# Kernel tuning notes

Hardware: AMD Instinct MI355X
Metric: run time of the kernel (lower is better)

The kernel has to match this reference:

```python
import jax, jax.numpy as jnp
import numpy as np

B, S, D = 4, 1024, 1024
H, DH = 16, 64          # num_heads, attention_dim_per_head = attention_dim // num_heads
BIAS_DIM = 64
N_BIAS = 16384          # number of sparse relative-bias entries
NEG_MIN = jnp.finfo(jnp.float32).min


def setup_inputs() -> dict:
    key = jax.random.key(0)
    ks = jax.random.split(key, 12)
    states = jax.random.normal(ks[0], (B, S, D), dtype=jnp.float32)
    key_states = jax.random.normal(ks[1], (B, S, D), dtype=jnp.float32)
    masks = jnp.ones((B, 1, S, S), dtype=jnp.float32)
    # attention_bias columns: (batch_idx, q_idx, k_idx, bias_id)
    bi = jax.random.randint(ks[2], (N_BIAS,), 0, B)
    qi = jax.random.randint(ks[3], (N_BIAS,), 0, S)
    ki = jax.random.randint(ks[4], (N_BIAS,), 0, S)
    ei = jax.random.randint(ks[5], (N_BIAS,), 0, BIAS_DIM)
    attention_bias = jnp.stack([bi, qi, ki, ei], axis=1).astype(jnp.int32)
    # glorot-ish scaled weights
    def glorot(k, shape, fan_in, fan_out):
        lim = np.sqrt(6.0 / (fan_in + fan_out))
        return jax.random.uniform(k, shape, jnp.float32, -lim, lim)
    Wq = glorot(ks[6], (D, H, DH), D, H * DH)
    Wk = glorot(ks[7], (D, H, DH), D, H * DH)
    Wv = glorot(ks[8], (D, H, DH), D, H * DH)
    Wo = glorot(ks[9], (H, DH, D), H * DH, D)
    bias_embs = glorot(ks[10], (BIAS_DIM, DH), BIAS_DIM, DH)
    bias_scalar = glorot(ks[11], (DH, 1), DH, 1)
    return {"states": states, "key_states": key_states, "masks": masks,
            "attention_bias": attention_bias, "Wq": Wq, "Wk": Wk, "Wv": Wv,
            "Wo": Wo, "bias_embs": bias_embs, "bias_scalar": bias_scalar}


def reference(states, key_states, masks, attention_bias, Wq, Wk, Wv, Wo, bias_embs, bias_scalar):
    # QKV projections: btd,dha->btha
    q = jnp.einsum('btd,dha->btha', states, Wq)
    k = jnp.einsum('btd,dha->btha', key_states, Wk)
    v = jnp.einsum('btd,dha->btha', key_states, Wv)
    # raw scores [B,H,Q,K]
    alpha = jnp.einsum('bkha,bqha->bhqk', k, q)
    # sparse relative bias: one_hot @ bias_embs == gather; @ bias_scalar -> scalar per entry
    k_red = jnp.sum(k, axis=-1)                                   # [B,K,H]
    bias_vals = (bias_embs[attention_bias[:, -1]] @ bias_scalar)[:, 0]  # [N]
    bqk = jnp.zeros((alpha.shape[0], alpha.shape[2], alpha.shape[3]), dtype=alpha.dtype)
    # tf.scatter_nd sums duplicate indices -> .at[...].add
    bqk = bqk.at[attention_bias[:, 0], attention_bias[:, 1], attention_bias[:, 2]].add(bias_vals)
    alpha = alpha + jnp.einsum('bqk,bkh->bhqk', bqk, k_red)
    alpha = alpha * jax.lax.rsqrt(jnp.float32(DH))
    alpha = alpha * masks + (1.0 - jnp.ceil(masks)) * NEG_MIN
    alpha = jax.nn.softmax(alpha, axis=-1)
    alpha = alpha * masks
    context = jnp.einsum('bhqk,bkha->bqha', alpha, v)
    return jnp.einsum('btha,had->btd', context, Wo)
```

## Files before the change

### kernel.cpp

```cpp
#include <hip/hip_runtime.h>
#include <stdint.h>


typedef __attribute__((ext_vector_type(8))) short short8;
typedef __attribute__((ext_vector_type(4))) float f32x4;
typedef __attribute__((ext_vector_type(4))) unsigned short ushort4v;
typedef __attribute__((ext_vector_type(2))) unsigned uint2v;
typedef __attribute__((ext_vector_type(4))) unsigned uint4v;

#define DEVI __device__ __forceinline__

constexpr float NEG_MIN = -3.4028234663852886e38f;
constexpr float LOG2E   = 1.4426950408889634f;

DEVI unsigned short f2b(float f) {
    union { float f; unsigned u; } x; x.f = f;
    unsigned u = x.u;
    unsigned r = (u + 0x7fffu + ((u >> 16) & 1u)) >> 16;
    return (unsigned short)r;
}
DEVI float hi_as_f(unsigned p) { union { unsigned u; float f; } x; x.u = p & 0xffff0000u; return x.f; }
DEVI float lo_as_f(unsigned p) { union { unsigned u; float f; } x; x.u = p << 16; return x.f; }
DEVI float asf(unsigned u) { union { unsigned u; float f; } x; x.u = u; return x.f; }

DEVI void gl_lds16(const unsigned short* g, unsigned short* l) {
    __builtin_amdgcn_global_load_lds(
        (const __attribute__((address_space(1))) unsigned int*)g,
        (__attribute__((address_space(3))) unsigned int*)l, 16, 0, 0);
}

DEVI short8 ldswz(const unsigned short* base, int row, int slot) {
    return *reinterpret_cast<const short8*>(
        reinterpret_cast<const char*>(base) + row * 128 + (((slot ^ row) & 7) << 4));
}

__global__ void __launch_bounds__(256) prep_kernel(const float* __restrict__ s0,
                                                   const float* __restrict__ s1,
                                                   const float* __restrict__ Wq,
                                                   const float* __restrict__ Wk,
                                                   const float* __restrict__ Wv,
                                                   const float* __restrict__ Wo,
                                                   unsigned short* __restrict__ d0,
                                                   unsigned short* __restrict__ d1,
                                                   unsigned short* __restrict__ Wqt,
                                                   unsigned short* __restrict__ Wot) {
    __shared__ float t[64][65];
    int bid = blockIdx.x, tid = threadIdx.x;
    if (bid < 8192) {
        int i = bid * 256 + tid;
        const float* src = (i < 1024 * 1024) ? s0 : s1;
        unsigned short* dst = (i < 1024 * 1024) ? d0 : d1;
        int j = i & (1024 * 1024 - 1);
        float4 v = reinterpret_cast<const float4*>(src)[j];
        ushort4v o;
        o.x = f2b(v.x); o.y = f2b(v.y); o.z = f2b(v.z); o.w = f2b(v.w);
        reinterpret_cast<ushort4v*>(dst)[j] = o;
        return;
    }
    int wb = bid - 8192;
    int wi = wb >> 8, sub = wb & 255;
    const float* src = (wi == 0) ? Wq : ((wi == 1) ? Wk : ((wi == 2) ? Wv : Wo));
    unsigned short* dst = (wi == 3) ? Wot : (Wqt + (size_t)wi * 1024 * 1024);
    float scale = (wi == 0) ? 0.125f : 1.0f;
    const int R = 1024, C = 1024;
    int bc = sub & 15, br = sub >> 4;
    int r0 = tid >> 4, c4 = (tid & 15) << 2;
    for (int i = 0; i < 4; ++i) {
        int row = r0 + i * 16;
        float4 v = *reinterpret_cast<const float4*>(&src[(size_t)(br * 64 + row) * C + bc * 64 + c4]);
        t[row][c4] = v.x; t[row][c4 + 1] = v.y; t[row][c4 + 2] = v.z; t[row][c4 + 3] = v.w;
    }
    __syncthreads();
    int cr0 = tid >> 4, r4 = (tid & 15) << 2;
    for (int i = 0; i < 4; ++i) {
        int crow = cr0 + i * 16;
        ushort4v o;
        o.x = f2b(t[r4][crow] * scale); o.y = f2b(t[r4 + 1][crow] * scale);
        o.z = f2b(t[r4 + 2][crow] * scale); o.w = f2b(t[r4 + 3][crow] * scale);
        *reinterpret_cast<ushort4v*>(&dst[(size_t)(bc * 64 + crow) * R + br * 64 + r4]) = o;
    }
}

template <int OUT_F32, int DO_KRED>
DEVI void gemm128_body(const unsigned short* __restrict__ A,
                       const unsigned short* __restrict__ Bt,
                       void* __restrict__ Cv, int bm, int bn,
                       unsigned short* As, unsigned short* Bs,
                       float* __restrict__ kredT) {
    const int Kd = 1024, N = 1024;
    int tid = threadIdx.x, l = tid & 63, w = tid >> 6;
    int wm = w >> 1, wn = w & 1;
    int l15 = l & 15, l16 = l >> 4;
    f32x4 acc[4][4] = {};
    int lr = l >> 3, ls = l & 7;
    int gcol = ((ls ^ (lr & 7)) << 3);
    const unsigned short* Ag = A + (size_t)(bm * 128 + w * 8 + lr) * Kd + gcol;
    const unsigned short* Bg = Bt + (size_t)(bn * 128 + w * 8 + lr) * Kd + gcol;
    unsigned short* AsW = As + (w * 8) * 64;
    unsigned short* BsW = Bs + (w * 8) * 64;
    for (int kt = 0; kt < Kd; kt += 64) {
        __syncthreads();
#pragma unroll
        for (int i = 0; i < 4; ++i) {
            gl_lds16(Ag + kt + (size_t)(i * 32) * Kd, AsW + i * 32 * 64);
            gl_lds16(Bg + kt + (size_t)(i * 32) * Kd, BsW + i * 32 * 64);
        }
        __syncthreads();
#pragma unroll
        for (int h = 0; h < 2; ++h) {
            short8 af[4], bf[4];
#pragma unroll
            for (int m = 0; m < 4; ++m)
                af[m] = ldswz(As, wm * 64 + m * 16 + l15, h * 4 + l16);
#pragma unroll
            for (int n = 0; n < 4; ++n)
                bf[n] = ldswz(Bs, wn * 64 + n * 16 + l15, h * 4 + l16);
#pragma unroll
            for (int m = 0; m < 4; ++m)
#pragma unroll
                for (int n = 0; n < 4; ++n)
                    acc[m][n] = __builtin_amdgcn_mfma_f32_16x16x32_bf16(af[m], bf[n], acc[m][n], 0, 0, 0);
        }
    }
#pragma unroll
    for (int m = 0; m < 4; ++m)
#pragma unroll
        for (int n = 0; n < 4; ++n)
#pragma unroll
            for (int r = 0; r < 4; ++r) {
                int row = bm * 128 + wm * 64 + m * 16 + ((l >> 4) << 2) + r;
                int col = bn * 128 + wn * 64 + n * 16 + l15;
                float v = acc[m][n][r];
                if (OUT_F32) reinterpret_cast<float*>(Cv)[(size_t)row * N + col] = v;
                else reinterpret_cast<unsigned short*>(Cv)[(size_t)row * N + col] = f2b(v);
            }
    if (DO_KRED) {
        int hw = bn * 2 + wn;
#pragma unroll
        for (int m = 0; m < 4; ++m) {
            f32x4 rs = (acc[m][0] + acc[m][1]) + (acc[m][2] + acc[m][3]);
#pragma unroll
            for (int d = 1; d < 16; d <<= 1) {
                f32x4 t;
                t[0] = __shfl_xor(rs[0], d); t[1] = __shfl_xor(rs[1], d);
                t[2] = __shfl_xor(rs[2], d); t[3] = __shfl_xor(rs[3], d);
                rs += t;
            }
            if (l15 == 0) {
#pragma unroll
                for (int r = 0; r < 4; ++r) {
                    int row = bm * 128 + wm * 64 + m * 16 + ((l >> 4) << 2) + r;
                    kredT[((size_t)((row >> 10) * 16 + hw) << 10) + (row & 1023)] = rs[r] * 0.125f;
                }
            }
        }
    }
}

__global__ void __launch_bounds__(256) gemm_qkv(const unsigned short* __restrict__ Sb,
                                                const unsigned short* __restrict__ Kb,
                                                const unsigned short* __restrict__ W3,
                                                unsigned short* __restrict__ Qb,
                                                unsigned short* __restrict__ Kbf,
                                                unsigned short* __restrict__ Vb,
                                                float* __restrict__ kredT) {
    __shared__ unsigned short As[128 * 64];
    __shared__ unsigned short Bs[128 * 64];
    int g = blockIdx.x >> 8, sub = blockIdx.x & 255;
    const unsigned short* A = (g == 0) ? Sb : Kb;
    const unsigned short* Bt = W3 + (size_t)g * (1024 * 1024);
    unsigned short* C = (g == 0) ? Qb : ((g == 1) ? Kbf : Vb);
    if (g == 1)
        gemm128_body<0, 1>(A, Bt, C, sub >> 3, sub & 7, As, Bs, kredT);
    else
        gemm128_body<0, 0>(A, Bt, C, sub >> 3, sub & 7, As, Bs, nullptr);
}

__global__ void __launch_bounds__(256) gemm_wo(const unsigned short* __restrict__ A,
                                               const unsigned short* __restrict__ Bt,
                                               float* __restrict__ C) {
    __shared__ unsigned short As[128 * 64];
    __shared__ unsigned short Bs[128 * 64];
    gemm128_body<1, 0>(A, Bt, C, blockIdx.x >> 3, blockIdx.x & 7, As, Bs, nullptr);
}

__global__ void __launch_bounds__(256) zero_tv(float* __restrict__ bqkT,
                                               const unsigned short* __restrict__ V,
                                               unsigned short* __restrict__ Vt) {
    __shared__ unsigned short t[64][66];
    int bid = blockIdx.x, tid = threadIdx.x;
    if (bid < 4096) {
        float4 z = {0.f, 0.f, 0.f, 0.f};
        reinterpret_cast<float4*>(bqkT)[bid * 256 + tid] = z;
        return;
    }
    int vb = bid - 4096;
    int st = vb & 15, h = (vb >> 4) & 15, b = vb >> 8;
    int s = tid >> 2, c16 = (tid & 3) << 4;
    const unsigned short* src = V + ((size_t)((b * 1024 + st * 64 + s) * 16 + h)) * 64 + c16;
    short8 v0 = *reinterpret_cast<const short8*>(src);
    short8 v1 = *reinterpret_cast<const short8*>(src + 8);
    for (int j = 0; j < 8; ++j) {
        t[s][c16 + j] = (unsigned short)v0[j];
        t[s][c16 + 8 + j] = (unsigned short)v1[j];
    }
    __syncthreads();
    int a = tid >> 2, s16 = (tid & 3) << 4;
    short8 o0, o1;
    for (int j = 0; j < 8; ++j) {
        o0[j] = (short)t[s16 + j][a];
        o1[j] = (short)t[s16 + 8 + j][a];
    }
    unsigned short* dst = Vt + ((size_t)((b * 16 + h) * 64 + a)) * 1024 + st * 64 + s16;
    *reinterpret_cast<short8*>(dst) = o0;
    *reinterpret_cast<short8*>(dst + 8) = o1;
}

__global__ void __launch_bounds__(256) scatter_bias(const int* __restrict__ ab,
                                                    const float* __restrict__ embs,
                                                    const float* __restrict__ scal,
                                                    float* __restrict__ pk2f, int n) {
    __shared__ float tab[64];
    int tid = threadIdx.x;
    if (tid < 64) {
        float v = 0.f;
        for (int a = 0; a < 64; ++a) v += embs[tid * 64 + a] * scal[a];
        tab[tid] = v;
    }
    __syncthreads();
    int i = blockIdx.x * 256 + tid;
    if (i >= n) return;
    int4 e = *reinterpret_cast<const int4*>(&ab[i * 4]);
    size_t idx = (((size_t)(e.x * 16 + (e.z >> 6)) * 1024) + e.y) * 64 + (e.z & 63);
    atomicAdd(&pk2f[idx], tab[e.w]);
}

__global__ void __launch_bounds__(256) pack_T(const float* __restrict__ masks,
                                              unsigned* __restrict__ pk2) {
    __shared__ float mt[64][65];
    int bid = blockIdx.x;
    int qb = bid & 15, kt = (bid >> 4) & 15, b = bid >> 8;
    int tid = threadIdx.x;
    int ql = tid >> 2, c = tid & 3;
    const float* mrow = masks + ((size_t)(b * 1024 + qb * 64 + ql)) * 1024 + kt * 64 + c * 16;
#pragma unroll
    for (int j = 0; j < 4; ++j) {
        float4 v = *reinterpret_cast<const float4*>(mrow + j * 4);
        mt[ql][c * 16 + j * 4 + 0] = v.x; mt[ql][c * 16 + j * 4 + 1] = v.y;
        mt[ql][c * 16 + j * 4 + 2] = v.z; mt[ql][c * 16 + j * 4 + 3] = v.w;
    }
    __syncthreads();
    unsigned* orow = pk2 + (((size_t)(b * 16 + kt) * 1024) + qb * 64 + ql) * 64 + c * 16;
#pragma unroll
    for (int j = 0; j < 4; ++j) {
        uint4v bv = *reinterpret_cast<const uint4v*>(orow + j * 4);
        uint4v o;
        o.x = ((unsigned)f2b(mt[ql][c * 16 + j * 4 + 0]) << 16) | f2b(asf(bv.x));
        o.y = ((unsigned)f2b(mt[ql][c * 16 + j * 4 + 1]) << 16) | f2b(asf(bv.y));
        o.z = ((unsigned)f2b(mt[ql][c * 16 + j * 4 + 2]) << 16) | f2b(asf(bv.z));
        o.w = ((unsigned)f2b(mt[ql][c * 16 + j * 4 + 3]) << 16) | f2b(asf(bv.w));
        *reinterpret_cast<uint4v*>(orow + j * 4) = o;
    }
}

__global__ void __launch_bounds__(256, 4) attn_kernel(const unsigned short* __restrict__ Q,
                                                      const unsigned short* __restrict__ K,
                                                      const unsigned short* __restrict__ Vt,
                                                      const unsigned* __restrict__ pk2,
                                                      const float* __restrict__ kredT,
                                                      unsigned short* __restrict__ ctx) {
    __shared__ __align__(16) unsigned short Ks[64 * 64];
    __shared__ __align__(16) unsigned short Vs[64 * 64];
    __shared__ __align__(16) unsigned short p_s[4][16][72];

    int bid = blockIdx.x;
    int g = bid & 63, qb = bid >> 6;
    int b = g >> 4, h = g & 15;
    int tid = threadIdx.x, w = tid >> 6, l = tid & 63;
    int qbase = qb * 64 + w * 16;
    int l15 = l & 15, l16 = l >> 4, koff = l16 << 3;

    int srow = tid >> 3, sslot = tid & 7;
    int sbyte = srow * 128 + (((sslot ^ srow) & 7) << 4);

    const unsigned short* Kg = K + ((size_t)b << 20) + h * 64 + sslot * 8;
    const unsigned short* Vg = Vt + ((size_t)(b * 16 + h) << 16) + (size_t)srow * 1024 + sslot * 8;
    const unsigned* pkp = pk2 + ((size_t)b << 20) + (size_t)(qbase + l15) * 64 + (l16 << 2);
    const float* krp = kredT + ((size_t)(b * 16 + h) << 10);

    short8 qf0, qf1;
    {
        const unsigned short* qp = Q + ((size_t)((b * 1024 + qbase + l15) * 16 + h)) * 64 + koff;
        qf0 = *reinterpret_cast<const short8*>(qp);
        qf1 = *reinterpret_cast<const short8*>(qp + 32);
    }

    short8 kpre0 = *reinterpret_cast<const short8*>(Kg + (size_t)srow * 1024);
    short8 kpre1 = *reinterpret_cast<const short8*>(Kg + (size_t)(srow + 32) * 1024);
    short8 vpre0 = *reinterpret_cast<const short8*>(Vg);
    short8 vpre1 = *reinterpret_cast<const short8*>(Vg + (size_t)32 * 1024);
    uint4v pku[4];
#pragma unroll
    for (int n = 0; n < 4; ++n) pku[n] = *reinterpret_cast<const uint4v*>(pkp + n * 16);
    f32x4 kr4[4];
#pragma unroll
    for (int n = 0; n < 4; ++n)
        kr4[n] = *reinterpret_cast<const f32x4*>(&krp[n * 16 + (l16 << 2)]);

    float m_r = -INFINITY, l_r = 0.f;
    f32x4 O[4] = {};

    for (int kt = 0; kt < 16; ++kt) {
        int kbase = kt * 64;

        __syncthreads();
        *reinterpret_cast<short8*>(reinterpret_cast<char*>(Ks) + sbyte) = kpre0;
        *reinterpret_cast<short8*>(reinterpret_cast<char*>(Ks) + 32 * 128 + sbyte) = kpre1;
        *reinterpret_cast<short8*>(reinterpret_cast<char*>(Vs) + sbyte) = vpre0;
        *reinterpret_cast<short8*>(reinterpret_cast<char*>(Vs) + 32 * 128 + sbyte) = vpre1;
        __syncthreads();

        if (kt < 15) {
            int nb = kbase + 64;
            kpre0 = *reinterpret_cast<const short8*>(Kg + (size_t)(nb + srow) * 1024);
            kpre1 = *reinterpret_cast<const short8*>(Kg + (size_t)(nb + srow + 32) * 1024);
            vpre0 = *reinterpret_cast<const short8*>(Vg + nb);
            vpre1 = *reinterpret_cast<const short8*>(Vg + (size_t)32 * 1024 + nb);
        }

        f32x4 sacc[4] = {};
        __builtin_amdgcn_s_setprio(1);
#pragma unroll
        for (int n = 0; n < 4; ++n) {
            int rk = n * 16 + l15;
            short8 kf0 = ldswz(Ks, rk, l16);
            short8 kf1 = ldswz(Ks, rk, 4 + l16);
            sacc[n] = __builtin_amdgcn_mfma_f32_16x16x32_bf16(kf0, qf0, sacc[n], 0, 0, 0);
            sacc[n] = __builtin_amdgcn_mfma_f32_16x16x32_bf16(kf1, qf1, sacc[n], 0, 0, 0);
        }
        __builtin_amdgcn_s_setprio(0);

        float tmax = -INFINITY;
#pragma unroll
        for (int n = 0; n < 4; ++n)
#pragma unroll
            for (int r = 0; r < 4; ++r) {
                unsigned pv = pku[n][r];
                float mv = hi_as_f(pv);
                float bq = lo_as_f(pv);
                float v = fmaf(bq, kr4[n][r], sacc[n][r]) * mv;
                if (!(mv > 0.f)) v += NEG_MIN;
                sacc[n][r] = v;
                tmax = fmaxf(tmax, v);
            }
        if (kt < 15) {
            const unsigned* pn = pkp + (size_t)(kt + 1) * 65536;
#pragma unroll
            for (int n = 0; n < 4; ++n) pku[n] = *reinterpret_cast<const uint4v*>(pn + n * 16);
#pragma unroll
            for (int n = 0; n < 4; ++n)
                kr4[n] = *reinterpret_cast<const f32x4*>(&krp[kbase + 64 + n * 16 + (l16 << 2)]);
        }

        tmax = fmaxf(tmax, __shfl_xor(tmax, 16));
        tmax = fmaxf(tmax, __shfl_xor(tmax, 32));

        bool defer = __all(tmax - m_r <= 5.f);
        if (!defer) {
            float nm = fmaxf(m_r, tmax);
            float al = exp2f((m_r - nm) * LOG2E);
            m_r = nm;
            l_r *= al;
            float alr[4];
#pragma unroll
            for (int r = 0; r < 4; ++r) alr[r] = __shfl(al, l16 * 4 + r);
#pragma unroll
            for (int af = 0; af < 4; ++af)
#pragma unroll
                for (int r = 0; r < 4; ++r) O[af][r] *= alr[r];
        }

        float ps = 0.f;
#pragma unroll
        for (int n = 0; n < 4; ++n) {
            float p0 = exp2f((sacc[n][0] - m_r) * LOG2E);
            float p1 = exp2f((sacc[n][1] - m_r) * LOG2E);
            float p2 = exp2f((sacc[n][2] - m_r) * LOG2E);
            float p3 = exp2f((sacc[n][3] - m_r) * LOG2E);
            ps += (p0 + p1) + (p2 + p3);
            uint2v pk2v;
            asm("v_cvt_pk_bf16_f32 %0, %1, %2" : "=v"(pk2v.x) : "v"(p0), "v"(p1));
            asm("v_cvt_pk_bf16_f32 %0, %1, %2" : "=v"(pk2v.y) : "v"(p2), "v"(p3));
            *reinterpret_cast<uint2v*>(&p_s[w][l15][n * 16 + (l16 << 2)]) = pk2v;
        }

        ps += __shfl_xor(ps, 16);
        ps += __shfl_xor(ps, 32);
        l_r += ps;

        __builtin_amdgcn_s_setprio(1);
#pragma unroll
        for (int ks = 0; ks < 2; ++ks) {
            short8 pa = *reinterpret_cast<const short8*>(&p_s[w][l15][ks * 32 + koff]);
#pragma unroll
            for (int af = 0; af < 4; ++af) {
                short8 vb = ldswz(Vs, af * 16 + l15, ks * 4 + l16);
                O[af] = __builtin_amdgcn_mfma_f32_16x16x32_bf16(pa, vb, O[af], 0, 0, 0);
            }
        }
        __builtin_amdgcn_s_setprio(0);
    }

    float llr[4];
#pragma unroll
    for (int r = 0; r < 4; ++r) llr[r] = __shfl(l_r, l16 * 4 + r);
#pragma unroll
    for (int af = 0; af < 4; ++af)
#pragma unroll
        for (int r = 0; r < 4; ++r) {
            int row = l16 * 4 + r;
            float v = O[af][r] / llr[r];
            ctx[((size_t)((b * 1024 + qbase + row) * 16 + h)) * 64 + af * 16 + l15] = f2b(v);
        }
}

extern "C" void kernel_launch(void* const* d_in, const int* in_sizes, int n_in,
                              void* d_out, int out_size, void* d_ws, size_t ws_size,
                              hipStream_t stream) {
    const float* states     = (const float*)d_in[0];
    const float* key_states = (const float*)d_in[1];
    const float* masks      = (const float*)d_in[2];
    const int*   ab         = (const int*)d_in[3];
    const float* Wq         = (const float*)d_in[4];
    const float* Wk         = (const float*)d_in[5];
    const float* Wv         = (const float*)d_in[6];
    const float* Wo         = (const float*)d_in[7];
    const float* embs       = (const float*)d_in[8];
    const float* scal       = (const float*)d_in[9];

    char* ws = (char*)d_ws;
    const size_t MB = 1024 * 1024;
    unsigned short* Sb   = (unsigned short*)(ws);
    unsigned short* Kb   = (unsigned short*)(ws + 8 * MB);
    float*          pk2f = (float*)(ws);
    unsigned short* Wqt  = (unsigned short*)(ws + 16 * MB);
    unsigned short* Wot  = (unsigned short*)(ws + 22 * MB);
    unsigned short* Qb   = (unsigned short*)(ws + 24 * MB);
    unsigned short* Kbf  = (unsigned short*)(ws + 32 * MB);
    unsigned short* Vb   = (unsigned short*)(ws + 40 * MB);
    unsigned short* ctx  = (unsigned short*)(ws + 40 * MB);
    unsigned short* Vt   = (unsigned short*)(ws + 48 * MB);
    float*          krdT = (float*)(ws + 56 * MB);
    (void)in_sizes; (void)n_in; (void)out_size; (void)ws_size;

    prep_kernel<<<9216, 256, 0, stream>>>(states, key_states, Wq, Wk, Wv, Wo, Sb, Kb, Wqt, Wot);

    gemm_qkv<<<768, 256, 0, stream>>>(Sb, Kb, Wqt, Qb, Kbf, Vb, krdT);

    zero_tv<<<5120, 256, 0, stream>>>(pk2f, Vb, Vt);
    scatter_bias<<<64, 256, 0, stream>>>(ab, embs, scal, pk2f, 16384);
    pack_T<<<1024, 256, 0, stream>>>(masks, (unsigned*)pk2f);

    attn_kernel<<<1024, 256, 0, stream>>>(Qb, Kbf, Vt, (const unsigned*)pk2f, krdT, ctx);

    gemm_wo<<<256, 256, 0, stream>>>(ctx, Wot, (float*)d_out);
}
```

Baseline: 157.0 us.

## Double-buffer K/V LDS tiles, swizzle P scratch, reorder block-to-head mapping

The K/V shared-memory tiles become double-buffered, so the barrier that guarded the overwrite at the top of each iteration is dropped and only one barrier per tile remains. The P staging buffer moves from padded rows to an XOR-swizzled 128-byte-row layout read through the same swizzled loader, which targets LDS bank conflicts. Block index decoding now puts batch in the low bits so neighbouring blocks share a head, and the setprio hints around the MFMA loops are removed. Doubling the K/V buffers raises LDS use per block, which can lower occupancy under the 4-blocks launch bound.

```diff
diff --git a/kernel.cpp b/kernel.cpp
--- a/kernel.cpp
+++ b/kernel.cpp
@@ -269,13 +269,13 @@
                                                       const unsigned* __restrict__ pk2,
                                                       const float* __restrict__ kredT,
                                                       unsigned short* __restrict__ ctx) {
-    __shared__ __align__(16) unsigned short Ks[64 * 64];
-    __shared__ __align__(16) unsigned short Vs[64 * 64];
-    __shared__ __align__(16) unsigned short p_s[4][16][72];
+    __shared__ __align__(16) unsigned short Ks[2][64 * 64];
+    __shared__ __align__(16) unsigned short Vs[2][64 * 64];
+    __shared__ __align__(16) unsigned short p_s[4][16 * 64];
 
     int bid = blockIdx.x;
     int g = bid & 63, qb = bid >> 6;
-    int b = g >> 4, h = g & 15;
+    int h = g >> 2, b = g & 3;
     int tid = threadIdx.x, w = tid >> 6, l = tid & 63;
     int qbase = qb * 64 + w * 16;
     int l15 = l & 15, l16 = l >> 4, koff = l16 << 3;
@@ -287,6 +287,10 @@
     const unsigned short* Vg = Vt + ((size_t)(b * 16 + h) << 16) + (size_t)srow * 1024 + sslot * 8;
     const unsigned* pkp = pk2 + ((size_t)b << 20) + (size_t)(qbase + l15) * 64 + (l16 << 2);
     const float* krp = kredT + ((size_t)(b * 16 + h) << 10);
+
+    char* psW = reinterpret_cast<char*>(&p_s[w][0]);
+    int ps_wr_base = l15 * 128 + ((l16 & 1) << 3);
+    int ps_wr_sw = l15 & 7;
 
     short8 qf0, qf1;
     {
@@ -309,15 +313,19 @@
 
     float m_r = -INFINITY, l_r = 0.f;
     f32x4 O[4] = {};
+    int cur = 0;
 
     for (int kt = 0; kt < 16; ++kt) {
         int kbase = kt * 64;
 
-        __syncthreads();
-        *reinterpret_cast<short8*>(reinterpret_cast<char*>(Ks) + sbyte) = kpre0;
-        *reinterpret_cast<short8*>(reinterpret_cast<char*>(Ks) + 32 * 128 + sbyte) = kpre1;
-        *reinterpret_cast<short8*>(reinterpret_cast<char*>(Vs) + sbyte) = vpre0;
-        *reinterpret_cast<short8*>(reinterpret_cast<char*>(Vs) + 32 * 128 + sbyte) = vpre1;
+        {
+            char* kb = reinterpret_cast<char*>(&Ks[cur][0]);
+            char* vb = reinterpret_cast<char*>(&Vs[cur][0]);
+            *reinterpret_cast<short8*>(kb + sbyte) = kpre0;
+            *reinterpret_cast<short8*>(kb + 32 * 128 + sbyte) = kpre1;
+            *reinterpret_cast<short8*>(vb + sbyte) = vpre0;
+            *reinterpret_cast<short8*>(vb + 32 * 128 + sbyte) = vpre1;
+        }
         __syncthreads();
 
         if (kt < 15) {
@@ -329,16 +337,14 @@
         }
 
         f32x4 sacc[4] = {};
-        __builtin_amdgcn_s_setprio(1);
 #pragma unroll
         for (int n = 0; n < 4; ++n) {
             int rk = n * 16 + l15;
-            short8 kf0 = ldswz(Ks, rk, l16);
-            short8 kf1 = ldswz(Ks, rk, 4 + l16);
+            short8 kf0 = ldswz(&Ks[cur][0], rk, l16);
+            short8 kf1 = ldswz(&Ks[cur][0], rk, 4 + l16);
             sacc[n] = __builtin_amdgcn_mfma_f32_16x16x32_bf16(kf0, qf0, sacc[n], 0, 0, 0);
             sacc[n] = __builtin_amdgcn_mfma_f32_16x16x32_bf16(kf1, qf1, sacc[n], 0, 0, 0);
         }
-        __builtin_amdgcn_s_setprio(0);
 
         float tmax = -INFINITY;
 #pragma unroll
@@ -391,24 +397,24 @@
             uint2v pk2v;
             asm("v_cvt_pk_bf16_f32 %0, %1, %2" : "=v"(pk2v.x) : "v"(p0), "v"(p1));
             asm("v_cvt_pk_bf16_f32 %0, %1, %2" : "=v"(pk2v.y) : "v"(p2), "v"(p3));
-            *reinterpret_cast<uint2v*>(&p_s[w][l15][n * 16 + (l16 << 2)]) = pk2v;
+            int slot = n * 2 + (l16 >> 1);
+            *reinterpret_cast<uint2v*>(psW + ps_wr_base + (((slot ^ ps_wr_sw) & 7) << 4)) = pk2v;
         }
 
         ps += __shfl_xor(ps, 16);
         ps += __shfl_xor(ps, 32);
         l_r += ps;
 
-        __builtin_amdgcn_s_setprio(1);
 #pragma unroll
         for (int ks = 0; ks < 2; ++ks) {
-            short8 pa = *reinterpret_cast<const short8*>(&p_s[w][l15][ks * 32 + koff]);
+            short8 pa = ldswz(&p_s[w][0], l15, ks * 4 + l16);
 #pragma unroll
             for (int af = 0; af < 4; ++af) {
-                short8 vb = ldswz(Vs, af * 16 + l15, ks * 4 + l16);
+                short8 vb = ldswz(&Vs[cur][0], af * 16 + l15, ks * 4 + l16);
                 O[af] = __builtin_amdgcn_mfma_f32_16x16x32_bf16(pa, vb, O[af], 0, 0, 0);
             }
         }
-        __builtin_amdgcn_s_setprio(0);
+        cur ^= 1;
     }
 
     float llr[4];
```

New measurement: 157.7 us. Within noise of the previous version (+0.4%).
